# Kernel optimization log

Measured on AMD Instinct MI355X. Metric: run time of the kernel, lower is better.

The kernel has to match this reference:

```python
import jax, jax.numpy as jnp
import numpy as np

B, S, D, VOCAB = 64, 2048, 256, 288

def setup_inputs() -> dict:
    key = jax.random.key(0)
    k1, k2, k3 = jax.random.split(key, 3)
    TE = jax.random.randint(k1, (B, S, 2), 0, VOCAB, dtype=jnp.int64)
    W1 = jax.random.normal(k2, (VOCAB + 7, D), dtype=jnp.float32) * 0.05
    b1 = jnp.zeros((D,), dtype=jnp.float32)
    W2 = jax.random.normal(k3, (D, D), dtype=jnp.float32) * 0.05
    b2 = jnp.zeros((D,), dtype=jnp.float32)
    return {"TE": TE, "T": VOCAB, "W1": W1, "b1": b1, "W2": W2, "b2": b2}

def reference(TE, T, W1, b1, W2, b2):
    # one_hot(day,7)||one_hot(time,T) @ W1  ==  gather rows of W1 and add
    day = TE[..., 0].astype(jnp.int32) % 7          # [B, S]
    tod = TE[..., 1].astype(jnp.int32) % T          # [B, S]
    h = W1[day] + W1[7 + tod] + b1                  # [B, S, D]  (Linear 1)
    h = jax.nn.relu(h)
    out = jnp.einsum('bsd,de->bse', h, W2) + b2     # [B, S, D]  (Linear 2)
    return out[:, :, None, :]                       # [B, S, 1, D]
```

## Files before the change

### kernel.cpp

```cpp
#include <hip/hip_runtime.h>
#include <hip/hip_bf16.h>


typedef __bf16 bf16x4 __attribute__((ext_vector_type(4)));
typedef __bf16 bf16x8 __attribute__((ext_vector_type(8)));
typedef float  f32x4  __attribute__((ext_vector_type(4)));

#define M_TOTAL   131072
#define BM        128


__global__ __launch_bounds__(64) void prep_all(const float* __restrict__ W1,
                                               const float* __restrict__ b1,
                                               const float* __restrict__ W2,
                                               __bf16* __restrict__ W2S,
                                               __bf16* __restrict__ Htab,
                                               const int* __restrict__ TE32,
                                               int* __restrict__ flag, int T) {
    const int b = blockIdx.x, lane = threadIdx.x;
    const int nTab = 7 * T;
    if (b < nTab) {
        const float* __restrict__ wa = W1 + (b / T) * 256;
        const float* __restrict__ wb = W1 + (7 + b % T) * 256;
        f32x4 a = *(const f32x4*)(wa + lane * 4);
        f32x4 c = *(const f32x4*)(wb + lane * 4);
        f32x4 d = *(const f32x4*)(b1 + lane * 4);
        bf16x4 h;
#pragma unroll
        for (int j = 0; j < 4; ++j) h[j] = (__bf16)fmaxf(a[j] + c[j] + d[j], 0.0f);
        *(bf16x4*)(Htab + b * 256 + lane * 4) = h;
    } else {
        const int wb = b - nTab;
#pragma unroll
        for (int q = 0; q < 2; ++q) {
            int c = (wb * 64 + lane) * 2 + q;
            int l = c & 63, ksnt = c >> 6;
            int ks = ksnt & 7, nt = ksnt >> 3;
            int n  = nt * 16 + (l & 15);
            int k0 = ks * 32 + (l >> 4) * 8;
            bf16x8 w;
#pragma unroll
            for (int j = 0; j < 8; ++j) w[j] = (__bf16)W2[(k0 + j) * 256 + n];
            *(bf16x8*)(W2S + c * 8) = w;
        }
        if (wb == 0) {
            int v = 0;
            for (int i = lane; i < 2048; i += 64) v |= TE32[2 * i + 1];
            unsigned long long nz = __ballot(v != 0);
            if (lane == 0) *flag = (nz == 0ull) ? 1 : 0;
        }
    }
}

__global__ __launch_bounds__(256, 3) void temb_gemm(
        const int*   __restrict__ TE32,
        const __bf16* __restrict__ Htab,
        const __bf16* __restrict__ W2S,
        const float* __restrict__ b2,
        const int*   __restrict__ flag,
        float* __restrict__ out, int T)
{
    __shared__ __bf16 Bs[4 * 8 * 512];

    const int is64 = *flag;
    const int tid  = threadIdx.x;
    const int wave = tid >> 6;
    const int lane = tid & 63;
    const int m    = lane & 15;
    const int quad = lane >> 4;
    const int rowBase = blockIdx.x * BM + wave * 32;

    int code[2];
#pragma unroll
    for (int t = 0; t < 2; ++t) {
        const int row = rowBase + t * 16 + m;
        int day, tod;
        if (is64) { int4 te = *(const int4*)(TE32 + 4 * row); day = te.x; tod = te.z; }
        else      { int2 te = *(const int2*)(TE32 + 2 * row); day = te.x; tod = te.y; }
        code[t] = (day % 7) * T + (tod % T);
    }
    bf16x8 hfrag[2][8];
#pragma unroll
    for (int t = 0; t < 2; ++t)
#pragma unroll
        for (int ks = 0; ks < 8; ++ks)
            hfrag[t][ks] = *(const bf16x8*)(Htab + code[t] * 256 + ks * 32 + quad * 8);

    const bf16x8* __restrict__ gsrc = (const bf16x8*)W2S + tid;
    bf16x8* __restrict__ ldst = (bf16x8*)Bs + tid;
    const bf16x8* __restrict__ lsrc = (const bf16x8*)Bs;

    bf16x8 stage[8];
#pragma unroll
    for (int q = 0; q < 8; ++q) stage[q] = gsrc[q * 256];

    for (int g = 0; g < 4; ++g) {
#pragma unroll
        for (int q = 0; q < 8; ++q) ldst[q * 256] = stage[q];
        __syncthreads();
        if (g < 3) {
#pragma unroll
            for (int q = 0; q < 8; ++q) stage[q] = gsrc[(g + 1) * 2048 + q * 256];
        }
#pragma unroll
        for (int ntl = 0; ntl < 4; ++ntl) {
            const int nt = g * 4 + ntl;
            f32x4 acc0 = {0.f, 0.f, 0.f, 0.f};
            f32x4 acc1 = {0.f, 0.f, 0.f, 0.f};
#pragma unroll
            for (int ks = 0; ks < 8; ++ks) {
                bf16x8 wfrag = lsrc[(ntl * 8 + ks) * 64 + lane];
                acc0 = __builtin_amdgcn_mfma_f32_16x16x32_bf16(wfrag, hfrag[0][ks], acc0, 0, 0, 0);
                acc1 = __builtin_amdgcn_mfma_f32_16x16x32_bf16(wfrag, hfrag[1][ks], acc1, 0, 0, 0);
            }
            const f32x4 bias = *(const f32x4*)(b2 + nt * 16 + quad * 4);
            f32x4 v0, v1;
#pragma unroll
            for (int r = 0; r < 4; ++r) { v0[r] = acc0[r] + bias[r]; v1[r] = acc1[r] + bias[r]; }
            float* p0 = out + (rowBase + m) * 256 + nt * 16 + quad * 4;
            *(f32x4*)p0 = v0;
            *(f32x4*)(p0 + 16 * 256) = v1;
        }
        __syncthreads();
    }
}

extern "C" void kernel_launch(void* const* d_in, const int* in_sizes, int n_in,
                              void* d_out, int out_size, void* d_ws, size_t ws_size,
                              hipStream_t stream) {
    const int*   TE = (const int*)  d_in[0];
    const float* W1 = (const float*)d_in[2];
    const float* b1 = (const float*)d_in[3];
    const float* W2 = (const float*)d_in[4];
    const float* b2 = (const float*)d_in[5];
    const int T = in_sizes[2] / 256 - 7;

    __bf16* W2S  = (__bf16*)d_ws;
    __bf16* Htab = (__bf16*)((char*)d_ws + 131072);
    int*    flag = (int*)((char*)d_ws + 131072 + (size_t)7 * T * 512);
    float*  out  = (float*)d_out;

    prep_all<<<7 * T + 64, 64, 0, stream>>>(W1, b1, W2, W2S, Htab, TE, flag, T);
    temb_gemm<<<M_TOTAL / BM, 256, 0, stream>>>(TE, Htab, W2S, b2, flag, out, T);
}
```

Before: 165.2 us.

## Precompute full output table per (day,tod) code and gather rows instead of GEMM

```diff
diff --git a/kernel.cpp b/kernel.cpp
--- a/kernel.cpp
+++ b/kernel.cpp
@@ -7,7 +7,6 @@
 typedef float  f32x4  __attribute__((ext_vector_type(4)));
 
 #define M_TOTAL   131072
-#define BM        128
 
 
 __global__ __launch_bounds__(64) void prep_all(const float* __restrict__ W1,
@@ -52,76 +51,72 @@
     }
 }
 
-__global__ __launch_bounds__(256, 3) void temb_gemm(
-        const int*   __restrict__ TE32,
+__global__ __launch_bounds__(256) void otab_gemm(
         const __bf16* __restrict__ Htab,
         const __bf16* __restrict__ W2S,
         const float* __restrict__ b2,
+        float* __restrict__ Otab, int T)
+{
+    const int wave = threadIdx.x >> 6;
+    const int lane = threadIdx.x & 63;
+    const int m    = lane & 15;
+    const int quad = lane >> 4;
+    const int rowBase = blockIdx.x * 128 + wave * 32;
+    const int nTab = 7 * T;
+
+    bf16x8 hfrag[2][8];
+#pragma unroll
+    for (int t = 0; t < 2; ++t) {
+        int row = rowBase + t * 16 + m;
+        if (row >= nTab) row = nTab - 1;
+#pragma unroll
+        for (int ks = 0; ks < 8; ++ks)
+            hfrag[t][ks] = *(const bf16x8*)(Htab + row * 256 + ks * 32 + quad * 8);
+    }
+#pragma unroll 4
+    for (int nt = 0; nt < 16; ++nt) {
+        f32x4 acc0 = {0.f, 0.f, 0.f, 0.f};
+        f32x4 acc1 = {0.f, 0.f, 0.f, 0.f};
+#pragma unroll
+        for (int ks = 0; ks < 8; ++ks) {
+            bf16x8 wfrag = *(const bf16x8*)(W2S + ((nt * 8 + ks) * 64 + lane) * 8);
+            acc0 = __builtin_amdgcn_mfma_f32_16x16x32_bf16(wfrag, hfrag[0][ks], acc0, 0, 0, 0);
+            acc1 = __builtin_amdgcn_mfma_f32_16x16x32_bf16(wfrag, hfrag[1][ks], acc1, 0, 0, 0);
+        }
+        const f32x4 bias = *(const f32x4*)(b2 + nt * 16 + quad * 4);
+        f32x4 v0, v1;
+#pragma unroll
+        for (int r = 0; r < 4; ++r) { v0[r] = acc0[r] + bias[r]; v1[r] = acc1[r] + bias[r]; }
+        float* p0 = Otab + (rowBase + m) * 256 + nt * 16 + quad * 4;
+        *(f32x4*)p0 = v0;
+        *(f32x4*)(p0 + 16 * 256) = v1;
+    }
+}
+
+__global__ __launch_bounds__(256, 8) void temb_copy(
+        const int*   __restrict__ TE32,
+        const float* __restrict__ Otab,
         const int*   __restrict__ flag,
         float* __restrict__ out, int T)
 {
-    __shared__ __bf16 Bs[4 * 8 * 512];
+    const int is64 = *flag;
+    const int wave = threadIdx.x >> 6;
+    const int lane = threadIdx.x & 63;
+    const int rowBase = blockIdx.x * 128 + wave * 32;
 
-    const int is64 = *flag;
-    const int tid  = threadIdx.x;
-    const int wave = tid >> 6;
-    const int lane = tid & 63;
-    const int m    = lane & 15;
-    const int quad = lane >> 4;
-    const int rowBase = blockIdx.x * BM + wave * 32;
-
-    int code[2];
-#pragma unroll
-    for (int t = 0; t < 2; ++t) {
-        const int row = rowBase + t * 16 + m;
+    int code = 0;
+    if (lane < 32) {
+        const int row = rowBase + lane;
         int day, tod;
         if (is64) { int4 te = *(const int4*)(TE32 + 4 * row); day = te.x; tod = te.z; }
         else      { int2 te = *(const int2*)(TE32 + 2 * row); day = te.x; tod = te.y; }
-        code[t] = (day % 7) * T + (tod % T);
+        code = (day % 7) * T + (tod % T);
     }
-    bf16x8 hfrag[2][8];
-#pragma unroll
-    for (int t = 0; t < 2; ++t)
-#pragma unroll
-        for (int ks = 0; ks < 8; ++ks)
-            hfrag[t][ks] = *(const bf16x8*)(Htab + code[t] * 256 + ks * 32 + quad * 8);
-
-    const bf16x8* __restrict__ gsrc = (const bf16x8*)W2S + tid;
-    bf16x8* __restrict__ ldst = (bf16x8*)Bs + tid;
-    const bf16x8* __restrict__ lsrc = (const bf16x8*)Bs;
-
-    bf16x8 stage[8];
-#pragma unroll
-    for (int q = 0; q < 8; ++q) stage[q] = gsrc[q * 256];
-
-    for (int g = 0; g < 4; ++g) {
-#pragma unroll
-        for (int q = 0; q < 8; ++q) ldst[q * 256] = stage[q];
-        __syncthreads();
-        if (g < 3) {
-#pragma unroll
-            for (int q = 0; q < 8; ++q) stage[q] = gsrc[(g + 1) * 2048 + q * 256];
-        }
-#pragma unroll
-        for (int ntl = 0; ntl < 4; ++ntl) {
-            const int nt = g * 4 + ntl;
-            f32x4 acc0 = {0.f, 0.f, 0.f, 0.f};
-            f32x4 acc1 = {0.f, 0.f, 0.f, 0.f};
-#pragma unroll
-            for (int ks = 0; ks < 8; ++ks) {
-                bf16x8 wfrag = lsrc[(ntl * 8 + ks) * 64 + lane];
-                acc0 = __builtin_amdgcn_mfma_f32_16x16x32_bf16(wfrag, hfrag[0][ks], acc0, 0, 0, 0);
-                acc1 = __builtin_amdgcn_mfma_f32_16x16x32_bf16(wfrag, hfrag[1][ks], acc1, 0, 0, 0);
-            }
-            const f32x4 bias = *(const f32x4*)(b2 + nt * 16 + quad * 4);
-            f32x4 v0, v1;
-#pragma unroll
-            for (int r = 0; r < 4; ++r) { v0[r] = acc0[r] + bias[r]; v1[r] = acc1[r] + bias[r]; }
-            float* p0 = out + (rowBase + m) * 256 + nt * 16 + quad * 4;
-            *(f32x4*)p0 = v0;
-            *(f32x4*)(p0 + 16 * 256) = v1;
-        }
-        __syncthreads();
+#pragma unroll 8
+    for (int r = 0; r < 32; ++r) {
+        const int c = __shfl(code, r);
+        const f32x4 v = *(const f32x4*)(Otab + c * 256 + lane * 4);
+        *(f32x4*)(out + (size_t)(rowBase + r) * 256 + lane * 4) = v;
     }
 }
 
@@ -135,11 +130,14 @@
     const float* b2 = (const float*)d_in[5];
     const int T = in_sizes[2] / 256 - 7;
 
-    __bf16* W2S  = (__bf16*)d_ws;
-    __bf16* Htab = (__bf16*)((char*)d_ws + 131072);
-    int*    flag = (int*)((char*)d_ws + 131072 + (size_t)7 * T * 512);
+    char* ws = (char*)d_ws;
+    __bf16* W2S  = (__bf16*)ws;
+    __bf16* Htab = (__bf16*)(ws + 131072);
+    float*  Otab = (float*) (ws + 131072 + (size_t)7 * T * 512);
+    int*    flag = (int*)   (ws + 131072 + (size_t)7 * T * 512 + 2048 * 1024);
     float*  out  = (float*)d_out;
 
     prep_all<<<7 * T + 64, 64, 0, stream>>>(W1, b1, W2, W2S, Htab, TE, flag, T);
-    temb_gemm<<<M_TOTAL / BM, 256, 0, stream>>>(TE, Htab, W2S, b2, flag, out, T);
+    otab_gemm<<<16, 256, 0, stream>>>(Htab, W2S, b2, Otab, T);
+    temb_copy<<<M_TOTAL / 128, 256, 0, stream>>>(TE, Otab, flag, out, T);
 }
```

New measurement: 192.3 us. +16.4%, slower.
